# Kernel optimization log

Measured on AMD Instinct MI355X. Metric: run time of the kernel, lower is better.

## Reference

```python
import jax, jax.numpy as jnp
import numpy as np

NUM, K = 5, 3
IN_DIM, D_OUT = 512, 512
N_U, BATCH, GATED_IN = 64, 8192, 576
NB = NUM + K + 1  # 9 basis channels (num+k splines + 1 SiLU base)
TERM_SIZES = (4, 8)
TERM_MULTS = (32768, 16384)  # 4*32768 + 8*16384 = 262144 = D_OUT*IN_DIM
WDIM = 128


def extend_grid(grid, k):
    # grid: (S, num+1) -> (S, num+1+2k), appending k knots each side with uniform spacing h
    h = (grid[:, -1:] - grid[:, :1]) / (grid.shape[1] - 1)
    left = grid[:, :1] + h * jnp.arange(-k, 0, dtype=grid.dtype)
    right = grid[:, -1:] + h * jnp.arange(1, k + 1, dtype=grid.dtype)
    return jnp.concatenate([left, grid, right], axis=1)


def B_batch(x, grid, k):
    # Cox-de-Boor recursion. x: (S, B), grid: (S, G) extended. Returns (S, G-k-1, B).
    xg = x[:, None, :]
    g = grid[:, :, None]
    v = ((xg >= g[:, :-1]) & (xg < g[:, 1:])).astype(x.dtype)
    for p in range(1, k + 1):
        v = (xg - g[:, :-(p + 1)]) / (g[:, p:-1] - g[:, :-(p + 1)]) * v[:, :-1] \
          + (g[:, p + 1:] - xg) / (g[:, p + 1:] - g[:, 1:-p]) * v[:, 1:]
    return v


def lazy_P(terms, mults, perm, w):
    # emlp-style lazy equivariant projector: permute rows, apply small block
    # projectors with multiplicities, un-permute. w: (R, C).
    invperm = jnp.argsort(perm)
    wp = w[perm]
    outs, off = [], 0
    for P, m in zip(terms, mults):
        s = P.shape[0]
        blk = wp[off:off + m * s].reshape(m, s, -1)
        outs.append(jnp.einsum('ij,mjc->mic', P, blk).reshape(m * s, -1))
        off += m * s
    return jnp.concatenate(outs, axis=0)[invperm]


def setup_inputs() -> dict:
    key = jax.random.key(0)
    ks = jax.random.split(key, 12)
    x = jax.random.normal(ks[0], (BATCH, GATED_IN), dtype=jnp.float32)
    grid = jnp.tile(jnp.linspace(-1.0, 1.0, NUM + 1, dtype=jnp.float32)[None, :], (N_U, 1))
    linear_weight = 0.05 * jax.random.normal(ks[1], (D_OUT, NB * IN_DIM), dtype=jnp.float32)
    linear_bias = 0.05 * jax.random.normal(ks[2], (D_OUT,), dtype=jnp.float32)
    P_term_a = 0.3 * jax.random.normal(ks[3], (TERM_SIZES[0], TERM_SIZES[0]), dtype=jnp.float32)
    P_term_b = 0.3 * jax.random.normal(ks[4], (TERM_SIZES[1], TERM_SIZES[1]), dtype=jnp.float32)
    Pb = (1.0 / np.sqrt(D_OUT)) * jax.random.normal(ks[5], (D_OUT, D_OUT), dtype=jnp.float32)
    bi_basis = 0.01 * jax.random.normal(ks[6], (WDIM, D_OUT, D_OUT), dtype=jnp.float32)
    bi_w = jax.random.normal(ks[7], (WDIM,), dtype=jnp.float32)
    u = jnp.sort(jax.random.randint(ks[8], (N_U,), 0, GATED_IN))
    indices = jax.random.randint(ks[9], (IN_DIM,), 0, N_U)
    perm = jax.random.permutation(ks[10], D_OUT * IN_DIM)
    return {"x": x, "grid": grid, "linear_weight": linear_weight, "linear_bias": linear_bias,
            "P_term_a": P_term_a, "P_term_b": P_term_b, "Pb": Pb,
            "bi_basis": bi_basis, "bi_w": bi_w, "u": u, "indices": indices, "perm": perm}


def reference(x, grid, linear_weight, linear_bias, P_term_a, P_term_b, Pb, bi_basis, bi_w, u, indices, perm):
    batch = x.shape[0]
    # gather gate scalars and build spline + base activations
    gs = x[:, u].T                                   # (S, B)
    eg = extend_grid(grid, K)                        # (S, num+1+2k)
    sp = B_batch(gs, eg, K)                          # (S, num+k, B)
    sp = jnp.transpose(sp, (2, 1, 0))                # (B, num+k, S)
    sb = jax.nn.silu(gs).T[:, None, :]               # (B, 1, S)
    g = jnp.concatenate([sp, sb], axis=1)            # (B, NB, S)
    g = g[:, :, indices]                             # (B, NB, in_dim) gather via inverse indices
    acts = (g * x[:, None, :IN_DIM]).reshape(batch, -1)  # (B, NB*in_dim)
    # equivariant weight projection
    w_r = linear_weight.reshape(D_OUT, NB, IN_DIM).transpose(0, 2, 1).reshape(D_OUT * IN_DIM, NB)
    W_r = lazy_P([P_term_a, P_term_b], TERM_MULTS, perm, w_r)
    W = W_r.reshape(D_OUT, IN_DIM, NB).transpose(0, 2, 1).reshape(D_OUT, NB * IN_DIM)
    b = Pb @ linear_bias
    out = acts @ W.T + b                             # (B, D_OUT)
    # bilinear equivariant mix
    bi_W = jnp.einsum('w,wij->ij', bi_w, bi_basis)   # (D_OUT, D_OUT)
    out = 0.1 * (out @ bi_W.T) + out
    return out
```

## Files before the change

kernel.cpp:

```cpp
#include <hip/hip_runtime.h>

#define DI __device__ __forceinline__

typedef __attribute__((ext_vector_type(8))) short short8;
typedef __attribute__((ext_vector_type(4))) float f32x4;

DI ushort f2bf(float f) {
  union { float f; unsigned u; } v; v.f = f;
  unsigned r = v.u + 0x7fffu + ((v.u >> 16) & 1u);
  return (ushort)(r >> 16);
}

DI void gload_lds16(const void* g, void* l) {
  __builtin_amdgcn_global_load_lds((const __attribute__((address_space(1))) void*)g,
                                   (__attribute__((address_space(3))) void*)l, 16, 0, 0);
}

__global__ __launch_bounds__(256) void k_biW(const float2* __restrict__ bb,
                                             const float* __restrict__ bw,
                                             float2* __restrict__ Mf32,
                                             uint* __restrict__ Mbf16) {
  __shared__ float w[128];
  int tid = threadIdx.x;
  if (tid < 128) w[tid] = bw[tid];
  __syncthreads();
  int t = blockIdx.x * 256 + tid;
  const float2* p = bb + t;
  float ax = 0.f, ay = 0.f;
#pragma unroll 8
  for (int k = 0; k < 128; ++k) {
    float2 v = p[(size_t)k * 131072];
    float s = w[k];
    ax += s * v.x; ay += s * v.y;
  }
  int i = t >> 8, j0 = (t & 255) * 2;
  float2 r;
  r.x = 0.1f * ax + (i == j0 + 0 ? 1.f : 0.f);
  r.y = 0.1f * ay + (i == j0 + 1 ? 1.f : 0.f);
  Mf32[t] = r;
  Mbf16[t] = (uint)f2bf(r.x) | ((uint)f2bf(r.y) << 16);
}

__global__ __launch_bounds__(256) void k_matvec(const float* __restrict__ A,
                                                const float* __restrict__ v,
                                                float* __restrict__ y) {
  int o = blockIdx.x * 4 + (threadIdx.x >> 6);
  int lane = threadIdx.x & 63;
  float acc = 0.f;
  for (int k = lane; k < 512; k += 64) acc += A[o * 512 + k] * v[k];
#pragma unroll
  for (int s = 32; s; s >>= 1) acc += __shfl_down(acc, s, 64);
  if (lane == 0) y[o] = acc;
}

__global__ __launch_bounds__(256) void k_lazyP(const float* __restrict__ LW,
                                               const float* __restrict__ Pa,
                                               const float* __restrict__ Pb8,
                                               const int* __restrict__ perm,
                                               ushort* __restrict__ Wt) {
  int q = blockIdx.x * 256 + threadIdx.x;
  int r = perm[q];
  int o = r >> 9, ic = r & 511;
  if (q < 131072) {
    int ii = q & 3;
    int base = q - ii;
    int r0 = perm[base], r1 = perm[base + 1], r2 = perm[base + 2], r3 = perm[base + 3];
    float p0 = Pa[ii * 4 + 0], p1 = Pa[ii * 4 + 1], p2 = Pa[ii * 4 + 2], p3 = Pa[ii * 4 + 3];
    int a0 = (r0 >> 9) * 4608 + (r0 & 511);
    int a1 = (r1 >> 9) * 4608 + (r1 & 511);
    int a2 = (r2 >> 9) * 4608 + (r2 & 511);
    int a3 = (r3 >> 9) * 4608 + (r3 & 511);
#pragma unroll
    for (int c = 0; c < 9; ++c) {
      int off = c * 512;
      float acc = p0 * LW[a0 + off] + p1 * LW[a1 + off] + p2 * LW[a2 + off] + p3 * LW[a3 + off];
      Wt[(size_t)(c * 512 + ic) * 512 + o] = f2bf(acc);
    }
  } else {
    int l2 = q - 131072;
    int ii = l2 & 7;
    int base = q - ii;
    int rr[8]; int aa[8]; float pp[8];
#pragma unroll
    for (int j = 0; j < 8; ++j) {
      rr[j] = perm[base + j];
      aa[j] = (rr[j] >> 9) * 4608 + (rr[j] & 511);
      pp[j] = Pb8[ii * 8 + j];
    }
#pragma unroll
    for (int c = 0; c < 9; ++c) {
      int off = c * 512;
      float acc = 0.f;
#pragma unroll
      for (int j = 0; j < 8; ++j) acc += pp[j] * LW[aa[j] + off];
      Wt[(size_t)(c * 512 + ic) * 512 + o] = f2bf(acc);
    }
  }
}

__global__ __launch_bounds__(256) void k_acts(const float* __restrict__ x,
                                              const float* __restrict__ grid,
                                              const int* __restrict__ u,
                                              const int* __restrict__ indices,
                                              ushort* __restrict__ acts) {
  __shared__ float basis[8][64][9];
  __shared__ int sidx[512];
  int tid = threadIdx.x;
  int b0 = blockIdx.x * 8;
  for (int i = tid; i < 512; i += 256) sidx[i] = indices[i];
#pragma unroll
  for (int e0 = 0; e0 < 2; ++e0) {
    int e = e0 * 256 + tid;
    int row = e >> 6, j = e & 63;
    float gs = x[(size_t)(b0 + row) * 576 + u[j]];
    float g0 = grid[j * 6], g5 = grid[j * 6 + 5];
    float h = (g5 - g0) * 0.2f;
    float lo = g0 - 3.f * h;
    float tt = (gs - lo) / h;
#pragma unroll
    for (int n = 0; n < 8; ++n) basis[row][j][n] = 0.f;
    float fc = floorf(tt);
    int c = (int)fc;
    if (c >= 0 && c <= 10) {
      float t = tt - fc;
      float t2 = t * t, t3 = t2 * t;
      float om = 1.f - t;
      float w0 = t3 * (1.f / 6.f);
      float w1 = (1.f + 3.f * t + 3.f * t2 - 3.f * t3) * (1.f / 6.f);
      float w2 = (4.f - 6.f * t2 + 3.f * t3) * (1.f / 6.f);
      float w3 = om * om * om * (1.f / 6.f);
      if (c <= 7) basis[row][j][c] = w0;
      if (c >= 1 && c <= 8) basis[row][j][c - 1] = w1;
      if (c >= 2 && c <= 9) basis[row][j][c - 2] = w2;
      if (c >= 3) basis[row][j][c - 3] = w3;
    }
    basis[row][j][8] = gs / (1.f + __expf(-gs));
  }
  __syncthreads();
#pragma unroll
  for (int rep = 0; rep < 2; ++rep) {
    int e = rep * 256 + tid;
    int row = e >> 6, i0 = (e & 63) * 8;
    size_t xb = (size_t)(b0 + row) * 576;
    float4 xa = *(const float4*)&x[xb + i0];
    float4 xc = *(const float4*)&x[xb + i0 + 4];
    int4 ja = *(const int4*)&sidx[i0];
    int4 jb = *(const int4*)&sidx[i0 + 4];
    size_t ab = (size_t)(b0 + row) * 4608 + i0;
#pragma unroll
    for (int n = 0; n < 9; ++n) {
      short8 hv;
      hv[0] = (short)f2bf(basis[row][ja.x][n] * xa.x);
      hv[1] = (short)f2bf(basis[row][ja.y][n] * xa.y);
      hv[2] = (short)f2bf(basis[row][ja.z][n] * xa.z);
      hv[3] = (short)f2bf(basis[row][ja.w][n] * xa.w);
      hv[4] = (short)f2bf(basis[row][jb.x][n] * xc.x);
      hv[5] = (short)f2bf(basis[row][jb.y][n] * xc.y);
      hv[6] = (short)f2bf(basis[row][jb.z][n] * xc.z);
      hv[7] = (short)f2bf(basis[row][jb.w][n] * xc.w);
      *(short8*)(&acts[ab + (size_t)n * 512]) = hv;
    }
  }
}

template <int BM, int BN, bool BIAS, bool OUTBF>
__global__ __launch_bounds__(256) void gemm_bt(const ushort* __restrict__ A,
                                               const ushort* __restrict__ B,
                                               void* __restrict__ Cout,
                                               const float* __restrict__ bias,
                                               int N, int Kd) {
  constexpr int BK = 64;
  constexpr int FM = BM / 32;
  constexpr int FN = BN / 32;
  __shared__ __align__(16) ushort Al[2][BM * BK];
  __shared__ __align__(16) ushort Bl[2][BN * BK];
  int tid = threadIdx.x, lane = tid & 63, wid = tid >> 6;
  int wm = wid >> 1, wn = wid & 1;
  int tiles_n = N / BN;
  int per_xcd = gridDim.x >> 3;
  int flat = (blockIdx.x & 7) * per_xcd + (blockIdx.x >> 3);
  int bm = flat / tiles_n, bn = flat % tiles_n;
  long m0 = (long)bm * BM;
  long n0 = (long)bn * BN;

  int swc = ((tid & 7) ^ ((tid >> 3) & 7)) * 8;
  const ushort* agp = A + (m0 + (tid >> 3)) * (long)Kd + swc;
  const ushort* bgp = B + (n0 + (tid >> 3)) * (long)Kd + swc;

#define STAGE(buf, k0)                                                        \
  do {                                                                        \
    _Pragma("unroll")                                                         \
    for (int it = 0; it < BM / 32; ++it)                                      \
      gload_lds16(agp + (it * 32) * (long)Kd + (k0), &Al[buf][(it * 256 + tid) * 8]); \
    _Pragma("unroll")                                                         \
    for (int it = 0; it < BN / 32; ++it)                                      \
      gload_lds16(bgp + (it * 32) * (long)Kd + (k0), &Bl[buf][(it * 256 + tid) * 8]); \
  } while (0)

  f32x4 acc[FM][FN] = {};
  int swz = (lane & 7) << 3;
  int nt = Kd / BK;
  STAGE(0, 0);
  __syncthreads();
  for (int t = 0; t < nt; ++t) {
    int cur = t & 1;
    if (t + 1 < nt) STAGE(cur ^ 1, (t + 1) * BK);
#pragma unroll
    for (int ks = 0; ks < 2; ++ks) {
      int kidx = (ks * 32 + (lane >> 4) * 8) ^ swz;
      short8 a[FM], b[FN];
#pragma unroll
      for (int f = 0; f < FM; ++f)
        a[f] = *(const short8*)&Al[cur][(wm * (FM * 16) + f * 16 + (lane & 15)) * BK + kidx];
#pragma unroll
      for (int f = 0; f < FN; ++f)
        b[f] = *(const short8*)&Bl[cur][(wn * (FN * 16) + f * 16 + (lane & 15)) * BK + kidx];
#pragma unroll
      for (int i = 0; i < FM; ++i)
#pragma unroll
        for (int j = 0; j < FN; ++j)
          acc[i][j] = __builtin_amdgcn_mfma_f32_16x16x32_bf16(a[i], b[j], acc[i][j], 0, 0, 0);
    }
    __syncthreads();
  }
#undef STAGE
#pragma unroll
  for (int i = 0; i < FM; ++i)
#pragma unroll
    for (int j = 0; j < FN; ++j) {
      int row_b = wm * (FM * 16) + i * 16 + ((lane >> 4) * 4);
      long col = n0 + wn * (FN * 16) + j * 16 + (lane & 15);
      float bv = BIAS ? bias[col] : 0.f;
#pragma unroll
      for (int r = 0; r < 4; ++r) {
        long row = m0 + row_b + r;
        float v = acc[i][j][r] + bv;
        if (OUTBF) ((ushort*)Cout)[row * N + col] = f2bf(v);
        else       ((float*)Cout)[row * N + col] = v;
      }
    }
}

extern "C" void kernel_launch(void* const* d_in, const int* in_sizes, int n_in,
                              void* d_out, int out_size, void* d_ws, size_t ws_size,
                              hipStream_t stream) {
  const float* x        = (const float*)d_in[0];
  const float* grid     = (const float*)d_in[1];
  const float* LW       = (const float*)d_in[2];
  const float* lb       = (const float*)d_in[3];
  const float* Pa       = (const float*)d_in[4];
  const float* Pb8      = (const float*)d_in[5];
  const float* Pbm      = (const float*)d_in[6];
  const float* bi_basis = (const float*)d_in[7];
  const float* bi_w     = (const float*)d_in[8];
  const int*   u        = (const int*)d_in[9];
  const int*   indices  = (const int*)d_in[10];
  const int*   perm     = (const int*)d_in[11];
  float* out = (float*)d_out;
  char* ws = (char*)d_ws;

  float*  Mf32  = (float*)(ws + 0);
  ushort* Mbf16 = (ushort*)(ws + 1048576);
  float*  tvec  = (float*)(ws + 1572864);
  float*  b2    = (float*)(ws + 1576960);
  ushort* Wt    = (ushort*)(ws + 2097152);
  ushort* W2    = (ushort*)(ws + 6815744);
  ushort* acts  = (ushort*)(ws + 11534336);

  k_biW<<<512, 256, 0, stream>>>((const float2*)bi_basis, bi_w, (float2*)Mf32, (uint*)Mbf16);
  k_matvec<<<128, 256, 0, stream>>>(Pbm, lb, tvec);
  k_matvec<<<128, 256, 0, stream>>>(Mf32, tvec, b2);
  k_lazyP<<<1024, 256, 0, stream>>>(LW, Pa, Pb8, perm, Wt);
  gemm_bt<128, 128, false, true><<<(512 / 128) * (4608 / 128), 256, 0, stream>>>(
      Mbf16, Wt, (void*)W2, nullptr, 4608, 512);
  k_acts<<<1024, 256, 0, stream>>>(x, grid, u, indices, acts);
  gemm_bt<128, 128, true, false><<<(8192 / 128) * (512 / 128), 256, 0, stream>>>(
      acts, W2, (void*)out, b2, 512, 4608);
}
```

Before: 187.7 us.

## Split-K the main GEMM into two halves and use shuffles in lazy projector

The big acts×W2 GEMM (8192×512×4608) previously launched only 256 tiles, about one per CU. It is now split along K into two halves, giving 512 blocks that write fp32 partials to the output and a workspace buffer. A new reduce kernel then sums the halves and adds the bias. The lazy-projector kernel now has each lane load only its own row's weight and gathers group members via wave shuffles, replacing redundant perm lookups and gathered global loads. This relies on permuted groups being contiguous within a wave, and the reduce pass adds extra fp32 traffic of about 32 MB.

```diff
diff --git a/kernel.cpp b/kernel.cpp
--- a/kernel.cpp
+++ b/kernel.cpp
@@ -59,40 +59,34 @@
                                                const int* __restrict__ perm,
                                                ushort* __restrict__ Wt) {
   int q = blockIdx.x * 256 + threadIdx.x;
+  int lane = threadIdx.x & 63;
   int r = perm[q];
   int o = r >> 9, ic = r & 511;
+  int a_own = o * 4608 + ic;
   if (q < 131072) {
-    int ii = q & 3;
-    int base = q - ii;
-    int r0 = perm[base], r1 = perm[base + 1], r2 = perm[base + 2], r3 = perm[base + 3];
-    float p0 = Pa[ii * 4 + 0], p1 = Pa[ii * 4 + 1], p2 = Pa[ii * 4 + 2], p3 = Pa[ii * 4 + 3];
-    int a0 = (r0 >> 9) * 4608 + (r0 & 511);
-    int a1 = (r1 >> 9) * 4608 + (r1 & 511);
-    int a2 = (r2 >> 9) * 4608 + (r2 & 511);
-    int a3 = (r3 >> 9) * 4608 + (r3 & 511);
+    int ii = lane & 3, g = lane & ~3;
+    float pp[4];
+#pragma unroll
+    for (int j = 0; j < 4; ++j) pp[j] = Pa[ii * 4 + j];
 #pragma unroll
     for (int c = 0; c < 9; ++c) {
-      int off = c * 512;
-      float acc = p0 * LW[a0 + off] + p1 * LW[a1 + off] + p2 * LW[a2 + off] + p3 * LW[a3 + off];
+      float v = LW[a_own + c * 512];
+      float acc = 0.f;
+#pragma unroll
+      for (int j = 0; j < 4; ++j) acc += pp[j] * __shfl(v, g + j, 64);
       Wt[(size_t)(c * 512 + ic) * 512 + o] = f2bf(acc);
     }
   } else {
-    int l2 = q - 131072;
-    int ii = l2 & 7;
-    int base = q - ii;
-    int rr[8]; int aa[8]; float pp[8];
-#pragma unroll
-    for (int j = 0; j < 8; ++j) {
-      rr[j] = perm[base + j];
-      aa[j] = (rr[j] >> 9) * 4608 + (rr[j] & 511);
-      pp[j] = Pb8[ii * 8 + j];
-    }
+    int ii = lane & 7, g = lane & ~7;
+    float pp[8];
+#pragma unroll
+    for (int j = 0; j < 8; ++j) pp[j] = Pb8[ii * 8 + j];
 #pragma unroll
     for (int c = 0; c < 9; ++c) {
-      int off = c * 512;
+      float v = LW[a_own + c * 512];
       float acc = 0.f;
 #pragma unroll
-      for (int j = 0; j < 8; ++j) acc += pp[j] * LW[aa[j] + off];
+      for (int j = 0; j < 8; ++j) acc += pp[j] * __shfl(v, g + j, 64);
       Wt[(size_t)(c * 512 + ic) * 512 + o] = f2bf(acc);
     }
   }
@@ -163,11 +157,10 @@
   }
 }
 
-template <int BM, int BN, bool BIAS, bool OUTBF>
+template <int BM, int BN>
 __global__ __launch_bounds__(256) void gemm_bt(const ushort* __restrict__ A,
                                                const ushort* __restrict__ B,
-                                               void* __restrict__ Cout,
-                                               const float* __restrict__ bias,
+                                               ushort* __restrict__ Cout,
                                                int N, int Kd) {
   constexpr int BK = 64;
   constexpr int FM = BM / 32;
@@ -182,7 +175,6 @@
   int bm = flat / tiles_n, bn = flat % tiles_n;
   long m0 = (long)bm * BM;
   long n0 = (long)bn * BN;
-
   int swc = ((tid & 7) ^ ((tid >> 3) & 7)) * 8;
   const ushort* agp = A + (m0 + (tid >> 3)) * (long)Kd + swc;
   const ushort* bgp = B + (n0 + (tid >> 3)) * (long)Kd + swc;
@@ -230,15 +222,96 @@
     for (int j = 0; j < FN; ++j) {
       int row_b = wm * (FM * 16) + i * 16 + ((lane >> 4) * 4);
       long col = n0 + wn * (FN * 16) + j * 16 + (lane & 15);
-      float bv = BIAS ? bias[col] : 0.f;
-#pragma unroll
-      for (int r = 0; r < 4; ++r) {
-        long row = m0 + row_b + r;
-        float v = acc[i][j][r] + bv;
-        if (OUTBF) ((ushort*)Cout)[row * N + col] = f2bf(v);
-        else       ((float*)Cout)[row * N + col] = v;
-      }
-    }
+#pragma unroll
+      for (int r = 0; r < 4; ++r)
+        Cout[(m0 + row_b + r) * N + col] = f2bf(acc[i][j][r]);
+    }
+}
+
+__global__ __launch_bounds__(256, 2) void gemm_sk(const ushort* __restrict__ A,
+                                                  const ushort* __restrict__ B,
+                                                  float* __restrict__ P0,
+                                                  float* __restrict__ P1) {
+  constexpr int BM = 128, BN = 128, BK = 64, FM = 4, FN = 4;
+  const int Kd = 4608, N = 512;
+  __shared__ __align__(16) ushort Al[2][BM * BK];
+  __shared__ __align__(16) ushort Bl[2][BN * BK];
+  int tid = threadIdx.x, lane = tid & 63, wid = tid >> 6;
+  int wm = wid >> 1, wn = wid & 1;
+  int per_xcd = gridDim.x >> 3;
+  int flat = (blockIdx.x & 7) * per_xcd + (blockIdx.x >> 3);
+  int kb = flat >> 8;
+  int rem = flat & 255;
+  int bm = rem >> 2, bn = rem & 3;
+  long m0 = (long)bm * BM;
+  long n0 = (long)bn * BN;
+  int kbase = kb * (Kd / 2);
+  float* Pout = kb ? P1 : P0;
+
+  int swc = ((tid & 7) ^ ((tid >> 3) & 7)) * 8;
+  const ushort* agp = A + (m0 + (tid >> 3)) * (long)Kd + kbase + swc;
+  const ushort* bgp = B + (n0 + (tid >> 3)) * (long)Kd + kbase + swc;
+
+#define STAGE(buf, k0)                                                        \
+  do {                                                                        \
+    _Pragma("unroll")                                                         \
+    for (int it = 0; it < 4; ++it)                                            \
+      gload_lds16(agp + (it * 32) * (long)Kd + (k0), &Al[buf][(it * 256 + tid) * 8]); \
+    _Pragma("unroll")                                                         \
+    for (int it = 0; it < 4; ++it)                                            \
+      gload_lds16(bgp + (it * 32) * (long)Kd + (k0), &Bl[buf][(it * 256 + tid) * 8]); \
+  } while (0)
+
+  f32x4 acc[FM][FN] = {};
+  int swz = (lane & 7) << 3;
+  const int nt = (Kd / 2) / BK;
+  STAGE(0, 0);
+  __syncthreads();
+  for (int t = 0; t < nt; ++t) {
+    int cur = t & 1;
+    if (t + 1 < nt) STAGE(cur ^ 1, (t + 1) * BK);
+#pragma unroll
+    for (int ks = 0; ks < 2; ++ks) {
+      int kidx = (ks * 32 + (lane >> 4) * 8) ^ swz;
+      short8 a[FM], b[FN];
+#pragma unroll
+      for (int f = 0; f < FM; ++f)
+        a[f] = *(const short8*)&Al[cur][(wm * 64 + f * 16 + (lane & 15)) * BK + kidx];
+#pragma unroll
+      for (int f = 0; f < FN; ++f)
+        b[f] = *(const short8*)&Bl[cur][(wn * 64 + f * 16 + (lane & 15)) * BK + kidx];
+#pragma unroll
+      for (int i = 0; i < FM; ++i)
+#pragma unroll
+        for (int j = 0; j < FN; ++j)
+          acc[i][j] = __builtin_amdgcn_mfma_f32_16x16x32_bf16(a[i], b[j], acc[i][j], 0, 0, 0);
+    }
+    __syncthreads();
+  }
+#undef STAGE
+#pragma unroll
+  for (int i = 0; i < FM; ++i)
+#pragma unroll
+    for (int j = 0; j < FN; ++j) {
+      int row_b = wm * 64 + i * 16 + ((lane >> 4) * 4);
+      long col = n0 + wn * 64 + j * 16 + (lane & 15);
+#pragma unroll
+      for (int r = 0; r < 4; ++r)
+        Pout[(m0 + row_b + r) * N + col] = acc[i][j][r];
+    }
+}
+
+__global__ __launch_bounds__(256) void k_reduce(float4* __restrict__ P0,
+                                                const float4* __restrict__ P1,
+                                                const float4* __restrict__ b2) {
+  int t = blockIdx.x * 256 + threadIdx.x;
+#pragma unroll
+  for (int rep = 0; rep < 2; ++rep) {
+    int e = rep * 524288 + t;
+    float4 a = P0[e], b = P1[e], c = b2[e & 127];
+    a.x += b.x + c.x; a.y += b.y + c.y; a.z += b.z + c.z; a.w += b.w + c.w;
+    P0[e] = a;
+  }
 }
 
 extern "C" void kernel_launch(void* const* d_in, const int* in_sizes, int n_in,
@@ -266,14 +339,15 @@
   ushort* Wt    = (ushort*)(ws + 2097152);
   ushort* W2    = (ushort*)(ws + 6815744);
   ushort* acts  = (ushort*)(ws + 11534336);
+  float*  P1    = (float*)(ws + 87031808);
 
   k_biW<<<512, 256, 0, stream>>>((const float2*)bi_basis, bi_w, (float2*)Mf32, (uint*)Mbf16);
   k_matvec<<<128, 256, 0, stream>>>(Pbm, lb, tvec);
   k_matvec<<<128, 256, 0, stream>>>(Mf32, tvec, b2);
   k_lazyP<<<1024, 256, 0, stream>>>(LW, Pa, Pb8, perm, Wt);
-  gemm_bt<128, 128, false, true><<<(512 / 128) * (4608 / 128), 256, 0, stream>>>(
-      Mbf16, Wt, (void*)W2, nullptr, 4608, 512);
+  gemm_bt<128, 128><<<(512 / 128) * (4608 / 128), 256, 0, stream>>>(
+      Mbf16, Wt, W2, 4608, 512);
   k_acts<<<1024, 256, 0, stream>>>(x, grid, u, indices, acts);
-  gemm_bt<128, 128, true, false><<<(8192 / 128) * (512 / 128), 256, 0, stream>>>(
-      acts, W2, (void*)out, b2, 512, 4608);
-}
+  gemm_sk<<<512, 256, 0, stream>>>(acts, W2, out, P1);
+  k_reduce<<<2048, 256, 0, stream>>>((float4*)out, (const float4*)P1, (const float4*)b2);
+}
```

Measured after the change: 167.2 us. -10.9%, faster.
